# Performance work log

Hardware: AMD Instinct MI355X
Metric: run time of the kernel (lower is better)

Reference implementation:

```python
import jax, jax.numpy as jnp
import numpy as np

B, S, L, D, H = 4, 4, 1024, 1024, 16  # batch, state_size, seq_len, d_model, num_heads
DEPTH = D // H
NEG = -1.0e9


def setup_inputs() -> dict:
    key = jax.random.key(0)
    ks = jax.random.split(key, 10)
    scale = 1.0 / np.sqrt(D)
    q = jax.random.normal(ks[0], (B, S, L, D), jnp.float32)
    k = jax.random.normal(ks[1], (B, S, L, D), jnp.float32)
    v = jax.random.normal(ks[2], (B, S, L, D), jnp.float32)
    mask = (jax.random.uniform(ks[3], (B, S, L, L)) < 0.1).astype(jnp.float32)
    wq = jax.random.normal(ks[4], (D, D), jnp.float32) * scale
    wk = jax.random.normal(ks[5], (D, D), jnp.float32) * scale
    wv = jax.random.normal(ks[6], (D, D), jnp.float32) * scale
    wo = jax.random.normal(ks[7], (D, D), jnp.float32) * scale
    bq = jnp.zeros((D,), jnp.float32)
    bk = jnp.zeros((D,), jnp.float32)
    bv = jnp.zeros((D,), jnp.float32)
    bo = jnp.zeros((D,), jnp.float32)
    return {"q": q, "k": k, "v": v, "mask": mask, "wq": wq, "bq": bq,
            "wk": wk, "bk": bk, "wv": wv, "bv": bv, "wo": wo, "bo": bo}


def _split_heads(x):
    # [B,S,L,D] -> [B,S,H,L,depth]
    b, s, l, _ = x.shape
    return x.reshape(b, s, l, H, DEPTH).transpose(0, 1, 3, 2, 4)


def reference(q, k, v, mask, wq, bq, wk, bk, wv, bv, wo, bo):
    qh = _split_heads(q @ wq + bq)
    kh = _split_heads(k @ wk + bk)
    vh = _split_heads(v @ wv + bv)
    # scaled dot-product attention, logits: [B,S,H,Lq,Lk]
    logits = jnp.einsum('bshqd,bshkd->bshqk', qh, kh) / jnp.sqrt(
        jnp.asarray(DEPTH, jnp.float32))
    logits = logits + mask[:, :, None, :, :] * NEG
    attn = jax.nn.softmax(logits, axis=-1)
    ctx = jnp.einsum('bshqk,bshkd->bshqd', attn, vh)
    # merge heads: [B,S,H,L,depth] -> [B,S,L,D]
    ctx = ctx.transpose(0, 1, 3, 2, 4).reshape(q.shape[0], q.shape[1], q.shape[2], D)
    out = ctx @ wo + bo
    attn_mean = attn.mean(axis=2)  # mean over heads -> [B,S,Lq,Lk]
    return out, attn_mean
```

## Files before the change

### kernel.cpp

```cpp
#include <hip/hip_runtime.h>

typedef _Float16 h16;
typedef _Float16 v8h __attribute__((ext_vector_type(8)));
typedef float    v4f __attribute__((ext_vector_type(4)));
typedef unsigned long long u64;

constexpr float QPRESCALE = 0.18033688f;

#define MFMA16(a,b,c) __builtin_amdgcn_mfma_f32_16x16x32_f16((a),(b),(c),0,0,0)

__device__ __forceinline__ float fexp2(float x) {
#if __has_builtin(__builtin_amdgcn_exp2f)
    return __builtin_amdgcn_exp2f(x);
#else
    return __expf(x * 0.69314718056f);
#endif
}
__device__ __forceinline__ float flog2(float x) {
#if __has_builtin(__builtin_amdgcn_logf)
    return __builtin_amdgcn_logf(x);
#else
    return __logf(x) * 1.44269504f;
#endif
}

__device__ __forceinline__ void gld16(const h16* g, const h16* l)
{
    __builtin_amdgcn_global_load_lds(
        (const __attribute__((address_space(1))) void*)g,
        (__attribute__((address_space(3))) void*)l, 16, 0, 0);
}

__global__ __launch_bounds__(256)
void cvt16(const float* __restrict__ x, h16* __restrict__ y)
{
    size_t i = ((size_t)blockIdx.x * 256 + threadIdx.x) * 4;
    float4 v = *(const float4*)(x + i);
    h16 o[4] = {(h16)v.x, (h16)v.y, (h16)v.z, (h16)v.w};
    *(uint2*)(y + i) = *(const uint2*)o;
}

__global__ __launch_bounds__(256)
void mkbits(const float* __restrict__ mask, u64* __restrict__ mb)
{
    size_t i = (size_t)blockIdx.x * 256 + threadIdx.x;
    float v = mask[i];
    u64 b = __ballot(v != 0.0f);
    if ((threadIdx.x & 63) == 0) mb[i >> 6] = b;
}

__global__ __launch_bounds__(256)
void wtrans(const float* __restrict__ W, h16* __restrict__ WT)
{
    __shared__ float Ts[64][65];
    const int tid = threadIdx.x;
    const int n0 = blockIdx.x * 64, k0 = blockIdx.y * 64;
    #pragma unroll
    for (int i = 0; i < 4; ++i) {
        int f = tid + i * 256; int r = f >> 4, c = (f & 15) * 4;
        float4 v = *(const float4*)(W + (size_t)(k0 + r) * 1024 + n0 + c);
        Ts[r][c] = v.x; Ts[r][c+1] = v.y; Ts[r][c+2] = v.z; Ts[r][c+3] = v.w;
    }
    __syncthreads();
    #pragma unroll
    for (int i = 0; i < 4; ++i) {
        int f = tid + i * 256; int r = f >> 4, c = (f & 15) * 4;
        h16 o[4];
        #pragma unroll
        for (int j = 0; j < 4; ++j) o[j] = (h16)Ts[c + j][r];
        *(uint2*)(WT + (size_t)(n0 + r) * 1024 + k0 + c) = *(const uint2*)o;
    }
}

__global__ __launch_bounds__(256)
void proj(const h16* __restrict__ A, const h16* __restrict__ BT,
          const float* __restrict__ bias, void* __restrict__ out, int mode)
{
    __shared__ h16 As[128 * 32];
    __shared__ h16 Bs[128 * 32];
    const int tid  = threadIdx.x;
    const int lane = tid & 63, wv = tid >> 6;
    const int quad = lane >> 4, l16 = lane & 15;
    const int m0 = blockIdx.y * 128, n0 = blockIdx.x * 128;
    const int wm = (wv & 1) * 64, wn = (wv >> 1) * 64;
    const int sr = wv * 16 + (lane >> 2);
    const int sc = (lane & 3) * 8;
    v4f acc[4][4] = {};
    for (int k0 = 0; k0 < 1024; k0 += 32) {
        #pragma unroll
        for (int i = 0; i < 2; ++i) {
            int r = i * 64 + sr;
            gld16(A  + (size_t)(m0 + r) * 1024 + k0 + sc, &As[i * 2048 + wv * 512]);
            gld16(BT + (size_t)(n0 + r) * 1024 + k0 + sc, &Bs[i * 2048 + wv * 512]);
        }
        __syncthreads();
        v8h af[4], bf[4];
        #pragma unroll
        for (int t = 0; t < 4; ++t) {
            af[t] = *(v8h*)&As[(wm + t*16 + l16) * 32 + quad * 8];
            bf[t] = *(v8h*)&Bs[(wn + t*16 + l16) * 32 + quad * 8];
        }
        #pragma unroll
        for (int mt = 0; mt < 4; ++mt)
            #pragma unroll
            for (int nt = 0; nt < 4; ++nt)
                acc[mt][nt] = MFMA16(af[mt], bf[nt], acc[mt][nt]);
        __syncthreads();
    }
    #pragma unroll
    for (int mt = 0; mt < 4; ++mt) {
        int mbase = m0 + wm + mt*16 + quad*4;
        #pragma unroll
        for (int nt = 0; nt < 4; ++nt) {
            int n = n0 + wn + nt*16 + l16;
            float bv = bias[n];
            #pragma unroll
            for (int r = 0; r < 4; ++r) {
                float y = acc[mt][nt][r] + bv;
                if (mode == 0) y *= QPRESCALE;
                int mm = mbase + r;
                int bs = mm >> 10, l = mm & 1023, h = n >> 6, d = n & 63;
                if (mode <= 1)
                    ((h16*)out)[(((size_t)bs*16 + h) * 1024 + l) * 64 + d] = (h16)y;
                else if (mode == 2)
                    ((h16*)out)[(((size_t)bs*16 + h) * 64 + d) * 1024 + l] = (h16)y;
                else
                    ((float*)out)[(size_t)mm * 1024 + n] = y;
            }
        }
    }
}

__global__ __launch_bounds__(256, 3)
void attn_ctx(const h16* __restrict__ qh, const h16* __restrict__ kh,
              const h16* __restrict__ vt, const u64* __restrict__ mbits,
              h16* __restrict__ ctx, float* __restrict__ Lst)
{
    __shared__ h16 Qs[128][68];
    __shared__ h16 Ks[64][68];
    __shared__ h16 Vs[64][68];
    __shared__ h16 Ps[128][68];
    const int tid  = threadIdx.x;
    const int lane = tid & 63, wv = tid >> 6;
    const int quad = lane >> 4, l16 = lane & 15;
    const int orig = blockIdx.x + (blockIdx.y << 8);
    const int slot = orig >> 3;
    const int bsh  = (orig & 7) + ((slot >> 3) << 3);
    const int qb   = (slot & 7) << 7;
    const int bs = bsh >> 4, h = bsh & 15;
    const int qw = wv * 32;
    const int fr = tid >> 3, fc = (tid & 7) * 8;

    uint4 rK0 = *(const uint4*)(kh + ((size_t)bsh*1024 + fr     ) * 64 + fc);
    uint4 rK1 = *(const uint4*)(kh + ((size_t)bsh*1024 + fr + 32) * 64 + fc);
    uint4 rV0 = *(const uint4*)(vt + ((size_t)bsh*64 + fr     ) * 1024 + fc);
    uint4 rV1 = *(const uint4*)(vt + ((size_t)bsh*64 + fr + 32) * 1024 + fc);

    #pragma unroll
    for (int i = 0; i < 4; ++i) {
        int f = tid + i * 256; int r = f >> 3, c = (f & 7) * 8;
        *(uint4*)&Qs[r][c] = *(const uint4*)(qh + ((size_t)bsh*1024 + qb + r) * 64 + c);
    }
    v8h bones;
    {
        h16 o = (l16 == 0) ? (h16)1.0f : (h16)0.0f;
        #pragma unroll
        for (int j = 0; j < 8; ++j) bones[j] = o;
    }
    const u64* mrb = mbits + ((size_t)bs*1024 + qb + qw + quad*4) * 16;

    v4f accp[2][4] = {};
    v4f accs[2] = {};
    for (int kt = 0; kt < 16; ++kt) {
        __syncthreads();
        *(uint4*)&Ks[fr     ][fc] = rK0;
        *(uint4*)&Ks[fr + 32][fc] = rK1;
        *(uint4*)&Vs[fr     ][fc] = rV0;
        *(uint4*)&Vs[fr + 32][fc] = rV1;
        if (kt < 15) {
            rK0 = *(const uint4*)(kh + ((size_t)bsh*1024 + (kt+1)*64 + fr     ) * 64 + fc);
            rK1 = *(const uint4*)(kh + ((size_t)bsh*1024 + (kt+1)*64 + fr + 32) * 64 + fc);
            rV0 = *(const uint4*)(vt + ((size_t)bsh*64 + fr     ) * 1024 + (kt+1)*64 + fc);
            rV1 = *(const uint4*)(vt + ((size_t)bsh*64 + fr + 32) * 1024 + (kt+1)*64 + fc);
        }
        __syncthreads();
        v4f s[2][4] = {};
        #pragma unroll
        for (int kc = 0; kc < 2; ++kc) {
            v8h aq[2], bk[4];
            aq[0] = *(v8h*)&Qs[qw      + l16][kc*32 + quad*8];
            aq[1] = *(v8h*)&Qs[qw + 16 + l16][kc*32 + quad*8];
            #pragma unroll
            for (int nt = 0; nt < 4; ++nt)
                bk[nt] = *(v8h*)&Ks[nt*16 + l16][kc*32 + quad*8];
            #pragma unroll
            for (int mt = 0; mt < 2; ++mt)
                #pragma unroll
                for (int nt = 0; nt < 4; ++nt)
                    s[mt][nt] = MFMA16(aq[mt], bk[nt], s[mt][nt]);
        }
        #pragma unroll
        for (int mt = 0; mt < 2; ++mt)
            #pragma unroll
            for (int r = 0; r < 4; ++r) {
                int ql = qw + mt*16 + quad*4 + r;
                u64 m64 = mrb[(mt*16 + r) * 16 + kt];
                uint lo = (uint)(m64 >> l16);
                uint hi = (uint)(m64 >> (l16 + 32));
                #pragma unroll
                for (int nt = 0; nt < 4; ++nt) {
                    uint b = (((nt & 2) ? hi : lo) >> ((nt & 1) * 16)) & 1u;
                    float p = b ? 0.0f : fexp2(s[mt][nt][r]);
                    Ps[ql][nt*16 + l16] = (h16)p;
                }
            }
        __syncthreads();
        #pragma unroll
        for (int kc = 0; kc < 2; ++kc) {
            v8h ap[2], bv[4];
            ap[0] = *(v8h*)&Ps[qw      + l16][kc*32 + quad*8];
            ap[1] = *(v8h*)&Ps[qw + 16 + l16][kc*32 + quad*8];
            #pragma unroll
            for (int nt = 0; nt < 4; ++nt)
                bv[nt] = *(v8h*)&Vs[nt*16 + l16][kc*32 + quad*8];
            #pragma unroll
            for (int mt = 0; mt < 2; ++mt) {
                accs[mt] = MFMA16(ap[mt], bones, accs[mt]);
                #pragma unroll
                for (int nt = 0; nt < 4; ++nt)
                    accp[mt][nt] = MFMA16(ap[mt], bv[nt], accp[mt][nt]);
            }
        }
    }
    float lq[8];
    #pragma unroll
    for (int mt = 0; mt < 2; ++mt)
        #pragma unroll
        for (int r = 0; r < 4; ++r)
            lq[mt*4 + r] = accs[mt][r];
    if (l16 == 0) {
        #pragma unroll
        for (int j = 0; j < 8; ++j)
            Lst[(size_t)bsh*1024 + qb + qw + (j >> 2)*16 + quad*4 + (j & 3)]
                = flog2(lq[j]);
    }
    float rcp[8];
    #pragma unroll
    for (int j = 0; j < 8; ++j) {
        float l = __shfl(lq[j], quad * 16);
        rcp[j] = 1.0f / l;
    }
    #pragma unroll
    for (int mt = 0; mt < 2; ++mt)
        #pragma unroll
        for (int nt = 0; nt < 4; ++nt) {
            int dep = nt*16 + l16;
            #pragma unroll
            for (int r = 0; r < 4; ++r) {
                int ql = qw + mt*16 + quad*4 + r;
                float y = accp[mt][nt][r] * rcp[mt*4 + r];
                ctx[((size_t)bs*1024 + qb + ql) * 1024 + h*64 + dep] = (h16)y;
            }
        }
}

__global__ __launch_bounds__(256)
void attn_mean_k(const h16* __restrict__ qh, const h16* __restrict__ kh,
                 const u64* __restrict__ mbits, const float* __restrict__ Lst,
                 float* __restrict__ am)
{
    __shared__ h16 Qs[128][68];
    __shared__ h16 Ks[64][68];
    const int tid  = threadIdx.x;
    const int lane = tid & 63, wv = tid >> 6;
    const int quad = lane >> 4, l16 = lane & 15;
    const int orig = blockIdx.x + (blockIdx.y << 4) + (blockIdx.z << 7);
    const int slot = orig >> 3;
    const int bs   = ((orig & 7) << 1) + (slot >> 7);
    const int kt   = slot & 15;
    const int qb   = ((slot >> 4) & 7) << 7;
    const int qw = wv * 32;
    float acc[2][4][4] = {};
    for (int h = 0; h < 16; ++h) {
        const int bsh = bs * 16 + h;
        __syncthreads();
        #pragma unroll
        for (int i = 0; i < 4; ++i) {
            int f = tid + i * 256; int r = f >> 3, c = (f & 7) * 8;
            *(uint4*)&Qs[r][c] = *(const uint4*)(qh + ((size_t)bsh*1024 + qb + r) * 64 + c);
        }
        #pragma unroll
        for (int i = 0; i < 2; ++i) {
            int f = tid + i * 256; int r = f >> 3, c = (f & 7) * 8;
            *(uint4*)&Ks[r][c] = *(const uint4*)(kh + ((size_t)bsh*1024 + kt*64 + r) * 64 + c);
        }
        __syncthreads();
        v4f s[2][4] = {};
        #pragma unroll
        for (int kc = 0; kc < 2; ++kc) {
            v8h aq[2], bk[4];
            aq[0] = *(v8h*)&Qs[qw      + l16][kc*32 + quad*8];
            aq[1] = *(v8h*)&Qs[qw + 16 + l16][kc*32 + quad*8];
            #pragma unroll
            for (int nt = 0; nt < 4; ++nt)
                bk[nt] = *(v8h*)&Ks[nt*16 + l16][kc*32 + quad*8];
            #pragma unroll
            for (int mt = 0; mt < 2; ++mt)
                #pragma unroll
                for (int nt = 0; nt < 4; ++nt)
                    s[mt][nt] = MFMA16(aq[mt], bk[nt], s[mt][nt]);
        }
        float ll[8];
        #pragma unroll
        for (int mt = 0; mt < 2; ++mt)
            #pragma unroll
            for (int r = 0; r < 4; ++r)
                ll[mt*4+r] = Lst[(size_t)bsh*1024 + qb + qw + mt*16 + quad*4 + r];
        #pragma unroll
        for (int mt = 0; mt < 2; ++mt)
            #pragma unroll
            for (int nt = 0; nt < 4; ++nt)
                #pragma unroll
                for (int r = 0; r < 4; ++r)
                    acc[mt][nt][r] += fexp2(s[mt][nt][r] - ll[mt*4+r]);
    }
    #pragma unroll
    for (int mt = 0; mt < 2; ++mt)
        #pragma unroll
        for (int r = 0; r < 4; ++r) {
            int ql = qw + mt*16 + quad*4 + r;
            u64 m64 = mbits[((size_t)bs*1024 + qb + ql) * 16 + kt];
            uint lo = (uint)(m64 >> l16);
            uint hi = (uint)(m64 >> (l16 + 32));
            #pragma unroll
            for (int nt = 0; nt < 4; ++nt) {
                uint b = (((nt & 2) ? hi : lo) >> ((nt & 1) * 16)) & 1u;
                am[((size_t)bs*1024 + qb + ql) * 1024 + kt*64 + nt*16 + l16]
                    = b ? 0.0f : acc[mt][nt][r] * 0.0625f;
            }
        }
}

extern "C" void kernel_launch(void* const* d_in, const int* in_sizes, int n_in,
                              void* d_out, int out_size, void* d_ws, size_t ws_size,
                              hipStream_t stream)
{
    const float* q    = (const float*)d_in[0];
    const float* k    = (const float*)d_in[1];
    const float* v    = (const float*)d_in[2];
    const float* mask = (const float*)d_in[3];
    const float* wq   = (const float*)d_in[4];
    const float* bq   = (const float*)d_in[5];
    const float* wk   = (const float*)d_in[6];
    const float* bk   = (const float*)d_in[7];
    const float* wv   = (const float*)d_in[8];
    const float* bv   = (const float*)d_in[9];
    const float* wo   = (const float*)d_in[10];
    const float* bo   = (const float*)d_in[11];

    const size_t TEN = (size_t)16384 * 1024;
    char* w = (char*)d_ws;
    h16* qf  = (h16*)w;             w += TEN * 2;
    h16* kf  = (h16*)w;             w += TEN * 2;
    h16* vf  = (h16*)w;             w += TEN * 2;
    h16* wqT = (h16*)w;             w += (size_t)1024*1024*2;
    h16* wkT = (h16*)w;             w += (size_t)1024*1024*2;
    h16* wvT = (h16*)w;             w += (size_t)1024*1024*2;
    h16* woT = (h16*)w;             w += (size_t)1024*1024*2;
    h16* qhh = (h16*)w;             w += TEN * 2;
    h16* khh = (h16*)w;             w += TEN * 2;
    h16* vtt = (h16*)w;             w += TEN * 2;
    h16* ctx = (h16*)w;             w += TEN * 2;
    float* Lst = (float*)w;         w += (size_t)256 * 1024 * 4;
    u64* mbits = (u64*)w;

    float* out = (float*)d_out;
    float* am  = out + TEN;

    mkbits<<<65536, 256, 0, stream>>>(mask, mbits);
    cvt16<<<16384, 256, 0, stream>>>(q, qf);
    cvt16<<<16384, 256, 0, stream>>>(k, kf);
    cvt16<<<16384, 256, 0, stream>>>(v, vf);
    wtrans<<<dim3(16,16), 256, 0, stream>>>(wq, wqT);
    wtrans<<<dim3(16,16), 256, 0, stream>>>(wk, wkT);
    wtrans<<<dim3(16,16), 256, 0, stream>>>(wv, wvT);
    wtrans<<<dim3(16,16), 256, 0, stream>>>(wo, woT);
    proj<<<dim3(8,128), 256, 0, stream>>>(qf, wqT, bq, qhh, 0);
    proj<<<dim3(8,128), 256, 0, stream>>>(kf, wkT, bk, khh, 1);
    proj<<<dim3(8,128), 256, 0, stream>>>(vf, wvT, bv, vtt, 2);
    attn_ctx<<<dim3(256,8), 256, 0, stream>>>(qhh, khh, vtt, mbits, ctx, Lst);
    attn_mean_k<<<dim3(16,8,16), 256, 0, stream>>>(qhh, khh, mbits, Lst, am);
    proj<<<dim3(8,128), 256, 0, stream>>>(ctx, woT, bo, out, 3);
}
```

Before: 835.6 us.

## Batch prep, transpose and projection launches; add XCD-aware tile mapping and MFMA priority

Merges the three fp16 converts and the mask bit-packing into one prep kernel, the four weight transposes into one launch, and the Q/K/V projections into one grid indexed by blockIdx.y. The projection tiles are remapped so each XCD gets contiguous M rows, to improve L2 reuse of the A and B tiles. s_setprio is raised around the MFMA sections of attn_ctx. This removes launch overhead and tail gaps between small kernels; the mask packing now uses 4 bits per thread plus shuffles instead of ballot, which adds a few more instructions per element.

```diff
diff --git a/kernel.cpp b/kernel.cpp
--- a/kernel.cpp
+++ b/kernel.cpp
@@ -32,26 +32,42 @@
 }
 
 __global__ __launch_bounds__(256)
-void cvt16(const float* __restrict__ x, h16* __restrict__ y)
-{
-    size_t i = ((size_t)blockIdx.x * 256 + threadIdx.x) * 4;
-    float4 v = *(const float4*)(x + i);
-    h16 o[4] = {(h16)v.x, (h16)v.y, (h16)v.z, (h16)v.w};
-    *(uint2*)(y + i) = *(const uint2*)o;
+void prep(const float* __restrict__ q, const float* __restrict__ k,
+          const float* __restrict__ v, const float* __restrict__ mask,
+          h16* __restrict__ qf, h16* __restrict__ kf, h16* __restrict__ vf,
+          u64* __restrict__ mb)
+{
+    const int z = blockIdx.y;
+    size_t t = (size_t)blockIdx.x * 256 + threadIdx.x;
+    size_t i = t * 4;
+    if (z < 3) {
+        const float* x = (z == 0) ? q : (z == 1) ? k : v;
+        h16* y        = (z == 0) ? qf : (z == 1) ? kf : vf;
+        float4 vv = *(const float4*)(x + i);
+        h16 o[4] = {(h16)vv.x, (h16)vv.y, (h16)vv.z, (h16)vv.w};
+        *(uint2*)(y + i) = *(const uint2*)o;
+    } else {
+        float4 mv = *(const float4*)(mask + i);
+        uint b4 = (mv.x != 0.0f ? 1u : 0u) | (mv.y != 0.0f ? 2u : 0u)
+                | (mv.z != 0.0f ? 4u : 0u) | (mv.w != 0.0f ? 8u : 0u);
+        u64 w = (u64)b4 << ((t & 15) * 4);
+        w |= __shfl_xor(w, 1);
+        w |= __shfl_xor(w, 2);
+        w |= __shfl_xor(w, 4);
+        w |= __shfl_xor(w, 8);
+        if ((threadIdx.x & 15) == 0) mb[t >> 4] = w;
+    }
 }
 
 __global__ __launch_bounds__(256)
-void mkbits(const float* __restrict__ mask, u64* __restrict__ mb)
-{
-    size_t i = (size_t)blockIdx.x * 256 + threadIdx.x;
-    float v = mask[i];
-    u64 b = __ballot(v != 0.0f);
-    if ((threadIdx.x & 63) == 0) mb[i >> 6] = b;
-}
-
-__global__ __launch_bounds__(256)
-void wtrans(const float* __restrict__ W, h16* __restrict__ WT)
-{
+void wtrans4(const float* __restrict__ w0, const float* __restrict__ w1,
+             const float* __restrict__ w2, const float* __restrict__ w3,
+             h16* __restrict__ t0, h16* __restrict__ t1,
+             h16* __restrict__ t2, h16* __restrict__ t3)
+{
+    const int z = blockIdx.z;
+    const float* W = (z == 0) ? w0 : (z == 1) ? w1 : (z == 2) ? w2 : w3;
+    h16* WT        = (z == 0) ? t0 : (z == 1) ? t1 : (z == 2) ? t2 : t3;
     __shared__ float Ts[64][65];
     const int tid = threadIdx.x;
     const int n0 = blockIdx.x * 64, k0 = blockIdx.y * 64;
@@ -72,16 +88,19 @@
     }
 }
 
-__global__ __launch_bounds__(256)
-void proj(const h16* __restrict__ A, const h16* __restrict__ BT,
-          const float* __restrict__ bias, void* __restrict__ out, int mode)
+__device__ __forceinline__
+void proj_body(const h16* __restrict__ A, const h16* __restrict__ BT,
+               const float* __restrict__ bias, void* __restrict__ out,
+               int mode, int lin)
 {
     __shared__ h16 As[128 * 32];
     __shared__ h16 Bs[128 * 32];
     const int tid  = threadIdx.x;
     const int lane = tid & 63, wv = tid >> 6;
     const int quad = lane >> 4, l16 = lane & 15;
-    const int m0 = blockIdx.y * 128, n0 = blockIdx.x * 128;
+    const int xcd = lin & 7, slot = lin >> 3;
+    const int m0 = (xcd * 16 + (slot >> 3)) * 128;
+    const int n0 = (slot & 7) * 128;
     const int wm = (wv & 1) * 64, wn = (wv >> 1) * 64;
     const int sr = wv * 16 + (lane >> 2);
     const int sc = (lane & 3) * 8;
@@ -129,6 +148,30 @@
             }
         }
     }
+}
+
+__global__ __launch_bounds__(256)
+void proj3(const h16* __restrict__ qf, const h16* __restrict__ kf,
+           const h16* __restrict__ vf,
+           const h16* __restrict__ wqT, const h16* __restrict__ wkT,
+           const h16* __restrict__ wvT,
+           const float* __restrict__ bq, const float* __restrict__ bk,
+           const float* __restrict__ bv,
+           h16* __restrict__ qhh, h16* __restrict__ khh, h16* __restrict__ vtt)
+{
+    const int z = blockIdx.y;
+    const h16* A   = (z == 0) ? qf  : (z == 1) ? kf  : vf;
+    const h16* BT  = (z == 0) ? wqT : (z == 1) ? wkT : wvT;
+    const float* b = (z == 0) ? bq  : (z == 1) ? bk  : bv;
+    h16* o         = (z == 0) ? qhh : (z == 1) ? khh : vtt;
+    proj_body(A, BT, b, o, z, blockIdx.x);
+}
+
+__global__ __launch_bounds__(256)
+void projo(const h16* __restrict__ A, const h16* __restrict__ BT,
+           const float* __restrict__ bias, float* __restrict__ out)
+{
+    proj_body(A, BT, bias, out, 3, blockIdx.x);
 }
 
 __global__ __launch_bounds__(256, 3)
@@ -185,6 +228,7 @@
         }
         __syncthreads();
         v4f s[2][4] = {};
+        __builtin_amdgcn_s_setprio(1);
         #pragma unroll
         for (int kc = 0; kc < 2; ++kc) {
             v8h aq[2], bk[4];
@@ -199,6 +243,7 @@
                 for (int nt = 0; nt < 4; ++nt)
                     s[mt][nt] = MFMA16(aq[mt], bk[nt], s[mt][nt]);
         }
+        __builtin_amdgcn_s_setprio(0);
         #pragma unroll
         for (int mt = 0; mt < 2; ++mt)
             #pragma unroll
@@ -215,6 +260,7 @@
                 }
             }
         __syncthreads();
+        __builtin_amdgcn_s_setprio(1);
         #pragma unroll
         for (int kc = 0; kc < 2; ++kc) {
             v8h ap[2], bv[4];
@@ -231,6 +277,7 @@
                     accp[mt][nt] = MFMA16(ap[mt], bv[nt], accp[mt][nt]);
             }
         }
+        __builtin_amdgcn_s_setprio(0);
     }
     float lq[8];
     #pragma unroll
@@ -377,18 +424,11 @@
     float* out = (float*)d_out;
     float* am  = out + TEN;
 
-    mkbits<<<65536, 256, 0, stream>>>(mask, mbits);
-    cvt16<<<16384, 256, 0, stream>>>(q, qf);
-    cvt16<<<16384, 256, 0, stream>>>(k, kf);
-    cvt16<<<16384, 256, 0, stream>>>(v, vf);
-    wtrans<<<dim3(16,16), 256, 0, stream>>>(wq, wqT);
-    wtrans<<<dim3(16,16), 256, 0, stream>>>(wk, wkT);
-    wtrans<<<dim3(16,16), 256, 0, stream>>>(wv, wvT);
-    wtrans<<<dim3(16,16), 256, 0, stream>>>(wo, woT);
-    proj<<<dim3(8,128), 256, 0, stream>>>(qf, wqT, bq, qhh, 0);
-    proj<<<dim3(8,128), 256, 0, stream>>>(kf, wkT, bk, khh, 1);
-    proj<<<dim3(8,128), 256, 0, stream>>>(vf, wvT, bv, vtt, 2);
-    attn_ctx<<<dim3(256,8), 256, 0, stream>>>(qhh, khh, vtt, mbits, ctx, Lst);
-    attn_mean_k<<<dim3(16,8,16), 256, 0, stream>>>(qhh, khh, mbits, Lst, am);
-    proj<<<dim3(8,128), 256, 0, stream>>>(ctx, woT, bo, out, 3);
-}
+    prep<<<dim3(16384, 4), 256, 0, stream>>>(q, k, v, mask, qf, kf, vf, mbits);
+    wtrans4<<<dim3(16, 16, 4), 256, 0, stream>>>(wq, wk, wv, wo, wqT, wkT, wvT, woT);
+    proj3<<<dim3(1024, 3), 256, 0, stream>>>(qf, kf, vf, wqT, wkT, wvT,
+                                             bq, bk, bv, qhh, khh, vtt);
+    attn_ctx<<<dim3(256, 8), 256, 0, stream>>>(qhh, khh, vtt, mbits, ctx, Lst);
+    attn_mean_k<<<dim3(16, 8, 16), 256, 0, stream>>>(qhh, khh, mbits, Lst, am);
+    projo<<<1024, 256, 0, stream>>>(ctx, woT, bo, out);
+}
```

Result: faster. 762.2 us (-8.8%).
